# Kernel optimization log

Hardware: AMD Instinct MI355X
Metric: run time of the kernel (lower is better)

Reference implementation:

```python
import jax, jax.numpy as jnp
import numpy as np

N_NODES = 100000


def gcn_conv(x, W, b, src, dst, n):
    # PyG GCNConv: h = X @ W, add self-loops, symmetric normalization, scatter-add, + bias
    h = x @ W  # [N, out]
    loop = jnp.arange(n, dtype=src.dtype)
    src2 = jnp.concatenate([src, loop])
    dst2 = jnp.concatenate([dst, loop])
    ew = jnp.ones(src2.shape[0], dtype=h.dtype)
    deg = jax.ops.segment_sum(ew, dst2, num_segments=n)  # in-degree incl. self-loop
    dinv = jnp.where(deg > 0, jax.lax.rsqrt(deg), 0.0)
    norm = dinv[src2] * dinv[dst2]  # [E+N]
    msg = h[src2] * norm[:, None]  # gather + scale
    out = jax.ops.segment_sum(msg, dst2, num_segments=n)  # scatter-add
    return out + b


def setup_inputs() -> dict:
    key = jax.random.key(0)
    k1, k2, k3, k4, k5 = jax.random.split(key, 5)
    n, e = N_NODES, 3200000
    d_in, d_hid, d_out = 512, 16, 7
    x = jax.random.normal(k1, (n, d_in), dtype=jnp.float32)
    edge_index = jax.random.randint(k2, (2, e), 0, n, dtype=jnp.int64)
    W1 = jax.random.normal(k3, (d_in, d_hid), dtype=jnp.float32) / np.sqrt(d_in)
    b1 = jnp.zeros((d_hid,), dtype=jnp.float32)
    W2 = jax.random.normal(k4, (d_hid, d_out), dtype=jnp.float32) / np.sqrt(d_hid)
    b2 = jnp.zeros((d_out,), dtype=jnp.float32)
    return {"x": x, "edge_index": edge_index, "W1": W1, "b1": b1, "W2": W2, "b2": b2}


def reference(x, edge_index, W1, b1, W2, b2):
    n = x.shape[0]
    src, dst = edge_index[0], edge_index[1]
    h = jax.nn.relu(gcn_conv(x, W1, b1, src, dst, n))
    # dropout is identity in eval mode
    h = gcn_conv(h, W2, b2, src, dst, n)
    return jax.nn.log_softmax(h, axis=1)
```

## Files before the change

### kernel.cpp

```cpp
#include <hip/hip_runtime.h>
#include <math.h>

#define D_IN 512
#define F1   16
#define F2   7

#define BKT_SHIFT 8
#define PK_SHIFT  18
#define PK_MASK   ((1u << PK_SHIFT) - 1u)
#define A_CHUNK   8192
#define B_CAP     16384

typedef float vf4 __attribute__((ext_vector_type(4)));

__global__ __launch_bounds__(256) void binhist_kernel(const int* __restrict__ dst,
                                                      int* __restrict__ bucket_cnt,
                                                      int E, int NB) {
    __shared__ int lh[512];
    for (int i = threadIdx.x; i < 512; i += 256) lh[i] = 0;
    __syncthreads();
    int base = blockIdx.x * A_CHUNK;
#pragma unroll
    for (int i = 0; i < A_CHUNK / 256; ++i) {
        int t = base + i * 256 + threadIdx.x;
        if (t < E) {
            int d = __builtin_nontemporal_load(&dst[t]);
            atomicAdd(&lh[d >> BKT_SHIFT], 1);
        }
    }
    __syncthreads();
    for (int i = threadIdx.x; i < NB; i += 256) {
        int v = lh[i];
        if (v) atomicAdd(&bucket_cnt[i], v);
    }
}

__global__ __launch_bounds__(512) void bucketscan_kernel(const int* __restrict__ bucket_cnt,
                                                         int* __restrict__ bucket_base,
                                                         int* __restrict__ bucket_cursor,
                                                         int NB, int E) {
    __shared__ int sm[512];
    int tid = threadIdx.x;
    int v = (tid < NB) ? bucket_cnt[tid] : 0;
    sm[tid] = v;
    __syncthreads();
    for (int off = 1; off < 512; off <<= 1) {
        int t = (tid >= off) ? sm[tid - off] : 0;
        __syncthreads();
        sm[tid] += t;
        __syncthreads();
    }
    if (tid < NB) {
        int ex = sm[tid] - v;
        bucket_base[tid] = ex;
        bucket_cursor[tid] = ex;
    }
    if (tid == 0) bucket_base[NB] = E;
}

__global__ __launch_bounds__(256) void bin_kernel(const int* __restrict__ src,
                                                  const int* __restrict__ dst,
                                                  int* __restrict__ bucket_cursor,
                                                  unsigned int* __restrict__ binned,
                                                  int E, int NB) {
    __shared__ int lh[512];
    __shared__ int lbase[512];
    __shared__ int lcur[512];
    __shared__ int sdelta[512];
    __shared__ int sA[512], sB[512];
    __shared__ unsigned int rbuf[A_CHUNK];
    __shared__ int rdelta[A_CHUNK];
    int tid = threadIdx.x;
    for (int i = tid; i < 512; i += 256) lh[i] = 0;
    __syncthreads();

    int base = blockIdx.x * A_CHUNK;
    int dcache[A_CHUNK / 256];
    int scache[A_CHUNK / 256];
#pragma unroll
    for (int i = 0; i < A_CHUNK / 256; ++i) {
        int t = base + i * 256 + tid;
        int d = -1, s = 0;
        if (t < E) {
            d = __builtin_nontemporal_load(&dst[t]);
            s = __builtin_nontemporal_load(&src[t]);
            atomicAdd(&lh[d >> BKT_SHIFT], 1);
        }
        dcache[i] = d;
        scache[i] = s;
    }
    __syncthreads();

    for (int i = tid; i < 512; i += 256) sA[i] = lh[i];
    __syncthreads();
    int* psrc = sA; int* pdst = sB;
    for (int off = 1; off < 512; off <<= 1) {
        for (int i = tid; i < 512; i += 256)
            pdst[i] = psrc[i] + ((i >= off) ? psrc[i - off] : 0);
        __syncthreads();
        int* tmp = psrc; psrc = pdst; pdst = tmp;
    }
    for (int i = tid; i < 512; i += 256) {
        int ex = psrc[i] - lh[i];
        lbase[i] = ex;
        lcur[i] = ex;
    }
    __syncthreads();

    for (int b = tid; b < NB; b += 256) {
        int c = lh[b];
        int g = c ? atomicAdd(&bucket_cursor[b], c) : 0;
        sdelta[b] = g - lbase[b];
    }
    __syncthreads();

#pragma unroll
    for (int i = 0; i < A_CHUNK / 256; ++i) {
        int d = dcache[i];
        if (d >= 0) {
            int b = d >> BKT_SHIFT;
            int p = atomicAdd(&lcur[b], 1);
            rbuf[p] = (unsigned int)scache[i] | ((unsigned int)(d & 255) << PK_SHIFT);
            rdelta[p] = sdelta[b];
        }
    }
    __syncthreads();

    int total = min(A_CHUNK, E - base);
    for (int p = tid; p < total; p += 256)
        binned[rdelta[p] + p] = rbuf[p];
}

__global__ __launch_bounds__(256) void csr_kernel(const unsigned int* __restrict__ binned,
                                                  const int* __restrict__ bucket_base,
                                                  int* __restrict__ row_ptr,
                                                  int* __restrict__ row_end,
                                                  float* __restrict__ dinv,
                                                  int* __restrict__ adj, int n) {
    __shared__ int lh[256], lscan[256], lcur[256];
    __shared__ unsigned int rbuf[B_CAP];
    int b = blockIdx.x;
    int tid = threadIdx.x;
    int gbase = bucket_base[b];
    int gend  = bucket_base[b + 1];
    int m = gend - gbase;
    lh[tid] = 0;
    __syncthreads();
    for (int i = tid; i < m; i += 256) {
        unsigned int w = __builtin_nontemporal_load(&binned[gbase + i]);
        if (i < B_CAP) rbuf[i] = w;
        atomicAdd(&lh[w >> PK_SHIFT], 1);
    }
    __syncthreads();
    int v = lh[tid];
    lscan[tid] = v;
    __syncthreads();
    for (int off = 1; off < 256; off <<= 1) {
        int t = (tid >= off) ? lscan[tid - off] : 0;
        __syncthreads();
        lscan[tid] += t;
        __syncthreads();
    }
    int ex = lscan[tid] - v;
    int node = (b << BKT_SHIFT) + tid;
    if (node < n) {
        row_ptr[node] = gbase + ex;
        row_end[node] = gbase + ex + v;
        dinv[node] = rsqrtf((float)v + 1.0f);
    }
    lcur[tid] = ex;
    __syncthreads();
    for (int i = tid; i < m; i += 256) {
        unsigned int w = (i < B_CAP) ? rbuf[i] : binned[gbase + i];
        int d = (int)(w >> PK_SHIFT);
        int s = (int)(w & PK_MASK);
        int p = atomicAdd(&lcur[d], 1);
        adj[gbase + p] = s;
    }
}

__global__ __launch_bounds__(256, 2) void mm1_kernel(const float* __restrict__ x,
                                                     const float* __restrict__ W1,
                                                     const float* __restrict__ dinv,
                                                     float* __restrict__ h1s, int n) {
    int tid = threadIdx.x;
    int lane = tid & 63;
    int wid  = blockIdx.x * 4 + (tid >> 6);
    int nwaves = gridDim.x * 4;

    float wA[4][16], wB[4][16];
#pragma unroll
    for (int r = 0; r < 4; ++r) {
        const float4* ra = (const float4*)(W1 + (size_t)(4 * lane + r) * F1);
        const float4* rb = (const float4*)(W1 + (size_t)(256 + 4 * lane + r) * F1);
#pragma unroll
        for (int q = 0; q < 4; ++q) {
            float4 va = ra[q], vb = rb[q];
            wA[r][4 * q + 0] = va.x; wA[r][4 * q + 1] = va.y;
            wA[r][4 * q + 2] = va.z; wA[r][4 * q + 3] = va.w;
            wB[r][4 * q + 0] = vb.x; wB[r][4 * q + 1] = vb.y;
            wB[r][4 * q + 2] = vb.z; wB[r][4 * q + 3] = vb.w;
        }
    }

    int node = wid;
    if (node >= n) return;
    const float* xb = x + (size_t)node * D_IN;
    vf4 pA = *(const vf4*)(xb + 4 * lane);
    vf4 pB = *(const vf4*)(xb + 256 + 4 * lane);

    while (node < n) {
        vf4 xA = pA, xB = pB;
        int nx = node + nwaves;
        if (nx < n) {
            const float* xn = x + (size_t)nx * D_IN;
            pA = *(const vf4*)(xn + 4 * lane);
            pB = *(const vf4*)(xn + 256 + 4 * lane);
        }
        float acc[16];
#pragma unroll
        for (int f = 0; f < 16; ++f) acc[f] = 0.f;
#pragma unroll
        for (int r = 0; r < 4; ++r) {
            float ea = xA[r], eb = xB[r];
#pragma unroll
            for (int f = 0; f < 16; ++f) {
                acc[f] += ea * wA[r][f];
                acc[f] += eb * wB[r][f];
            }
        }
        int h0 = lane & 1, h1 = lane & 2, h2 = lane & 4, h3 = lane & 8;
        float a[8];
#pragma unroll
        for (int j = 0; j < 8; ++j) {
            float keep = h0 ? acc[2 * j + 1] : acc[2 * j];
            float give = h0 ? acc[2 * j] : acc[2 * j + 1];
            a[j] = keep + __shfl_xor(give, 1);
        }
        float b[4];
#pragma unroll
        for (int j = 0; j < 4; ++j) {
            float keep = h1 ? a[2 * j + 1] : a[2 * j];
            float give = h1 ? a[2 * j] : a[2 * j + 1];
            b[j] = keep + __shfl_xor(give, 2);
        }
        float c[2];
#pragma unroll
        for (int j = 0; j < 2; ++j) {
            float keep = h2 ? b[2 * j + 1] : b[2 * j];
            float give = h2 ? b[2 * j] : b[2 * j + 1];
            c[j] = keep + __shfl_xor(give, 4);
        }
        float d = (h3 ? c[1] : c[0]) + __shfl_xor(h3 ? c[0] : c[1], 8);
        d += __shfl_xor(d, 16);
        d += __shfl_xor(d, 32);
        if (lane < 16) {
            float di = dinv[node];
            h1s[(size_t)node * F1 + lane] = d * di;
        }
        node = nx;
    }
}

__global__ __launch_bounds__(256) void agg1_kernel(const int* __restrict__ row_ptr,
                                                   const int* __restrict__ row_end,
                                                   const int* __restrict__ adj,
                                                   const float* __restrict__ h,
                                                   const float* __restrict__ dinv,
                                                   const float* __restrict__ b1,
                                                   float* __restrict__ acc, int n) {
    int t = blockIdx.x * 256 + threadIdx.x;
    int node = t >> 4, j = t & 15;
    if (node >= n) return;
    int s = row_ptr[node], e = row_end[node];
    float a0 = 0.0f, a1 = 0.0f;
    int k = s;
    for (; k + 1 < e; k += 2) {
        int s0 = adj[k], s1 = adj[k + 1];
        a0 += h[(size_t)s0 * F1 + j];
        a1 += h[(size_t)s1 * F1 + j];
    }
    if (k < e) a0 += h[(size_t)adj[k] * F1 + j];
    float di = dinv[node];
    float v = di * (a0 + a1 + h[(size_t)node * F1 + j]) + b1[j];
    acc[(size_t)node * F1 + j] = v > 0.0f ? v : 0.0f;
}

__global__ __launch_bounds__(256) void mm2_kernel(const float* __restrict__ hin,
                                                  const float* __restrict__ W2,
                                                  const float* __restrict__ dinv,
                                                  float* __restrict__ h2s, int n) {
    int t = blockIdx.x * blockDim.x + threadIdx.x;
    if (t >= n) return;
    const float4* hr = (const float4*)(hin + (size_t)t * F1);
    float hv[F1];
#pragma unroll
    for (int q = 0; q < 4; ++q) {
        float4 v = hr[q];
        hv[4 * q + 0] = v.x; hv[4 * q + 1] = v.y;
        hv[4 * q + 2] = v.z; hv[4 * q + 3] = v.w;
    }
    float acc[F2];
#pragma unroll
    for (int j = 0; j < F2; ++j) acc[j] = 0.0f;
#pragma unroll
    for (int k = 0; k < F1; ++k) {
        float xv = hv[k];
#pragma unroll
        for (int j = 0; j < F2; ++j) acc[j] += xv * W2[k * F2 + j];
    }
    float di = dinv[t];
    float* outp = h2s + (size_t)t * 8;
#pragma unroll
    for (int j = 0; j < F2; ++j) outp[j] = acc[j] * di;
    outp[7] = 0.0f;
}

__global__ __launch_bounds__(256) void agg2_kernel(const int* __restrict__ row_ptr,
                                                   const int* __restrict__ row_end,
                                                   const int* __restrict__ adj,
                                                   const float* __restrict__ h,
                                                   const float* __restrict__ dinv,
                                                   const float* __restrict__ b2,
                                                   float* __restrict__ out, int n) {
    int t = blockIdx.x * 256 + threadIdx.x;
    int node = t >> 3, j = t & 7;
    if (node >= n) return;
    int s = row_ptr[node], e = row_end[node];
    float a0 = 0.0f, a1 = 0.0f;
    int k = s;
    for (; k + 1 < e; k += 2) {
        int s0 = adj[k], s1 = adj[k + 1];
        a0 += h[(size_t)s0 * 8 + j];
        a1 += h[(size_t)s1 * 8 + j];
    }
    if (k < e) a0 += h[(size_t)adj[k] * 8 + j];
    float di = dinv[node];
    float bj = j < F2 ? b2[j] : 0.0f;
    float v = di * (a0 + a1 + h[(size_t)node * 8 + j]) + bj;
    if (j >= F2) v = -INFINITY;
    float m = v;
#pragma unroll
    for (int w = 1; w < 8; w <<= 1) m = fmaxf(m, __shfl_xor(m, w, 8));
    float ex = (j < F2) ? expf(v - m) : 0.0f;
    float sum = ex;
#pragma unroll
    for (int w = 1; w < 8; w <<= 1) sum += __shfl_xor(sum, w, 8);
    float lse = m + logf(sum);
    if (j < F2) out[(size_t)node * F2 + j] = v - lse;
}

extern "C" void kernel_launch(void* const* d_in, const int* in_sizes, int n_in,
                              void* d_out, int out_size, void* d_ws, size_t ws_size,
                              hipStream_t stream) {
    const float* x  = (const float*)d_in[0];
    const int*   ei = (const int*)d_in[1];
    const float* W1 = (const float*)d_in[2];
    const float* b1 = (const float*)d_in[3];
    const float* W2 = (const float*)d_in[4];
    const float* b2 = (const float*)d_in[5];

    int n = in_sizes[0] / D_IN;
    int E = in_sizes[1] / 2;
    const int* src = ei;
    const int* dst = ei + E;
    int NB = (n + 255) >> BKT_SHIFT;

    char* ws = (char*)d_ws;
    size_t o = 0;
    int* bucket_cnt    = (int*)(ws + o); o += 512 * 4;
    int* bucket_base   = (int*)(ws + o); o += 516 * 4;
    int* bucket_cursor = (int*)(ws + o); o += 512 * 4;
    int*   row_ptr = (int*)(ws + o);   o += (size_t)n * 4;
    int*   row_end = (int*)(ws + o);   o += (size_t)n * 4;
    float* dinv    = (float*)(ws + o); o += (size_t)n * 4;
    int*   adj     = (int*)(ws + o);   o += (size_t)E * 4;
    size_t uni = (size_t)E > (size_t)n * 32 ? (size_t)E : (size_t)n * 32;
    unsigned int* binned = (unsigned int*)(ws + o);
    float* h1s  = (float*)(ws + o);
    float* acc1 = (float*)(ws + o) + (size_t)n * F1;
    o += uni * 4;
    float* h2s = h1s;
    float* out = (float*)d_out;

    const int B = 256;
    int GA = (E + A_CHUNK - 1) / A_CHUNK;
    int gN = (n + B - 1) / B;

    hipMemsetAsync(bucket_cnt, 0, 512 * sizeof(int), stream);

    binhist_kernel<<<GA, B, 0, stream>>>(dst, bucket_cnt, E, NB);
    bucketscan_kernel<<<1, 512, 0, stream>>>(bucket_cnt, bucket_base, bucket_cursor, NB, E);
    bin_kernel<<<GA, B, 0, stream>>>(src, dst, bucket_cursor, binned, E, NB);
    csr_kernel<<<NB, B, 0, stream>>>(binned, bucket_base, row_ptr, row_end, dinv, adj, n);

    mm1_kernel<<<512, B, 0, stream>>>(x, W1, dinv, h1s, n);

    agg1_kernel<<<((size_t)n * F1 + B - 1) / B, B, 0, stream>>>(row_ptr, row_end, adj, h1s, dinv, b1, acc1, n);

    mm2_kernel<<<gN, B, 0, stream>>>(acc1, W2, dinv, h2s, n);

    agg2_kernel<<<((size_t)n * 8 + B - 1) / B, B, 0, stream>>>(row_ptr, row_end, adj, h2s, dinv, b2, out, n);
}
```

Baseline: 500.9 us.

## Fuse layer-2 matmul into agg1 and vectorize neighbor gathers with float4

The layer-1 aggregation kernel now also applies bias, ReLU and the 16x7 W2 projection in registers, using lane shuffles to reduce partial products. The separate mm2 kernel and its intermediate buffer round trip are removed. Both aggregation kernels now split each node's edges across lane groups, with every lane loading a float4 slice of a neighbor row, followed by a shuffle reduction. This replaces scalar per-feature gathers and is meant to cut gather instruction count and raise memory-level parallelism. It costs extra shuffles, and lanes do uneven work when a node has few edges.

```diff
diff --git a/kernel.cpp b/kernel.cpp
--- a/kernel.cpp
+++ b/kernel.cpp
@@ -268,52 +268,58 @@
                                                    const float* __restrict__ h,
                                                    const float* __restrict__ dinv,
                                                    const float* __restrict__ b1,
-                                                   float* __restrict__ acc, int n) {
+                                                   const float* __restrict__ W2,
+                                                   float* __restrict__ h2s, int n) {
     int t = blockIdx.x * 256 + threadIdx.x;
-    int node = t >> 4, j = t & 15;
+    int node = t >> 4;
     if (node >= n) return;
+    int li = t & 15;
+    int jq = li & 3;
+    int e4 = li >> 2;
     int s = row_ptr[node], e = row_end[node];
-    float a0 = 0.0f, a1 = 0.0f;
-    int k = s;
-    for (; k + 1 < e; k += 2) {
-        int s0 = adj[k], s1 = adj[k + 1];
-        a0 += h[(size_t)s0 * F1 + j];
-        a1 += h[(size_t)s1 * F1 + j];
-    }
-    if (k < e) a0 += h[(size_t)adj[k] * F1 + j];
+    vf4 a0 = {0.f, 0.f, 0.f, 0.f}, a1 = {0.f, 0.f, 0.f, 0.f};
+    int k = s + e4;
+    for (; k + 4 < e; k += 8) {
+        int s0 = adj[k], s1 = adj[k + 4];
+        a0 += *(const vf4*)(h + (size_t)s0 * F1 + jq * 4);
+        a1 += *(const vf4*)(h + (size_t)s1 * F1 + jq * 4);
+    }
+    if (k < e) a0 += *(const vf4*)(h + (size_t)adj[k] * F1 + jq * 4);
+    vf4 sum = a0 + a1;
+#pragma unroll
+    for (int q = 0; q < 4; ++q) {
+        sum[q] += __shfl_xor(sum[q], 4, 16);
+        sum[q] += __shfl_xor(sum[q], 8, 16);
+    }
     float di = dinv[node];
-    float v = di * (a0 + a1 + h[(size_t)node * F1 + j]) + b1[j];
-    acc[(size_t)node * F1 + j] = v > 0.0f ? v : 0.0f;
-}
-
-__global__ __launch_bounds__(256) void mm2_kernel(const float* __restrict__ hin,
-                                                  const float* __restrict__ W2,
-                                                  const float* __restrict__ dinv,
-                                                  float* __restrict__ h2s, int n) {
-    int t = blockIdx.x * blockDim.x + threadIdx.x;
-    if (t >= n) return;
-    const float4* hr = (const float4*)(hin + (size_t)t * F1);
-    float hv[F1];
-#pragma unroll
-    for (int q = 0; q < 4; ++q) {
-        float4 v = hr[q];
-        hv[4 * q + 0] = v.x; hv[4 * q + 1] = v.y;
-        hv[4 * q + 2] = v.z; hv[4 * q + 3] = v.w;
-    }
-    float acc[F2];
-#pragma unroll
-    for (int j = 0; j < F2; ++j) acc[j] = 0.0f;
-#pragma unroll
-    for (int k = 0; k < F1; ++k) {
-        float xv = hv[k];
-#pragma unroll
-        for (int j = 0; j < F2; ++j) acc[j] += xv * W2[k * F2 + j];
-    }
-    float di = dinv[t];
-    float* outp = h2s + (size_t)t * 8;
-#pragma unroll
-    for (int j = 0; j < F2; ++j) outp[j] = acc[j] * di;
-    outp[7] = 0.0f;
+    vf4 self = *(const vf4*)(h + (size_t)node * F1 + jq * 4);
+    float v0 = di * (sum[0] + self[0]) + b1[jq * 4 + 0]; v0 = v0 > 0.f ? v0 : 0.f;
+    float v1 = di * (sum[1] + self[1]) + b1[jq * 4 + 1]; v1 = v1 > 0.f ? v1 : 0.f;
+    float v2 = di * (sum[2] + self[2]) + b1[jq * 4 + 2]; v2 = v2 > 0.f ? v2 : 0.f;
+    float v3 = di * (sum[3] + self[3]) + b1[jq * 4 + 3]; v3 = v3 > 0.f ? v3 : 0.f;
+    const float* w0 = W2 + (size_t)(jq * 4 + 0) * F2;
+    const float* w1 = W2 + (size_t)(jq * 4 + 1) * F2;
+    const float* w2 = W2 + (size_t)(jq * 4 + 2) * F2;
+    const float* w3 = W2 + (size_t)(jq * 4 + 3) * F2;
+    float p0 = v0 * w0[0] + v1 * w1[0] + v2 * w2[0] + v3 * w3[0];
+    float p1 = v0 * w0[1] + v1 * w1[1] + v2 * w2[1] + v3 * w3[1];
+    float p2 = v0 * w0[2] + v1 * w1[2] + v2 * w2[2] + v3 * w3[2];
+    float p3 = v0 * w0[3] + v1 * w1[3] + v2 * w2[3] + v3 * w3[3];
+    float p4 = v0 * w0[4] + v1 * w1[4] + v2 * w2[4] + v3 * w3[4];
+    float p5 = v0 * w0[5] + v1 * w1[5] + v2 * w2[5] + v3 * w3[5];
+    float p6 = v0 * w0[6] + v1 * w1[6] + v2 * w2[6] + v3 * w3[6];
+    p0 += __shfl_xor(p0, 1, 16); p0 += __shfl_xor(p0, 2, 16);
+    p1 += __shfl_xor(p1, 1, 16); p1 += __shfl_xor(p1, 2, 16);
+    p2 += __shfl_xor(p2, 1, 16); p2 += __shfl_xor(p2, 2, 16);
+    p3 += __shfl_xor(p3, 1, 16); p3 += __shfl_xor(p3, 2, 16);
+    p4 += __shfl_xor(p4, 1, 16); p4 += __shfl_xor(p4, 2, 16);
+    p5 += __shfl_xor(p5, 1, 16); p5 += __shfl_xor(p5, 2, 16);
+    p6 += __shfl_xor(p6, 1, 16); p6 += __shfl_xor(p6, 2, 16);
+    if (li < 8) {
+        float oc = li == 0 ? p0 : li == 1 ? p1 : li == 2 ? p2 : li == 3 ? p3
+                 : li == 4 ? p4 : li == 5 ? p5 : li == 6 ? p6 : 0.0f;
+        h2s[(size_t)node * 8 + li] = oc * di;
+    }
 }
 
 __global__ __launch_bounds__(256) void agg2_kernel(const int* __restrict__ row_ptr,
@@ -324,30 +330,40 @@
                                                    const float* __restrict__ b2,
                                                    float* __restrict__ out, int n) {
     int t = blockIdx.x * 256 + threadIdx.x;
-    int node = t >> 3, j = t & 7;
+    int node = t >> 3;
     if (node >= n) return;
+    int li = t & 7;
+    int jh = li & 1;
+    int e4 = li >> 1;
     int s = row_ptr[node], e = row_end[node];
-    float a0 = 0.0f, a1 = 0.0f;
-    int k = s;
-    for (; k + 1 < e; k += 2) {
-        int s0 = adj[k], s1 = adj[k + 1];
-        a0 += h[(size_t)s0 * 8 + j];
-        a1 += h[(size_t)s1 * 8 + j];
-    }
-    if (k < e) a0 += h[(size_t)adj[k] * 8 + j];
+    vf4 a0 = {0.f, 0.f, 0.f, 0.f}, a1 = {0.f, 0.f, 0.f, 0.f};
+    int k = s + e4;
+    for (; k + 4 < e; k += 8) {
+        int s0 = adj[k], s1 = adj[k + 4];
+        a0 += *(const vf4*)(h + (size_t)s0 * 8 + jh * 4);
+        a1 += *(const vf4*)(h + (size_t)s1 * 8 + jh * 4);
+    }
+    if (k < e) a0 += *(const vf4*)(h + (size_t)adj[k] * 8 + jh * 4);
+    vf4 sum = a0 + a1;
+#pragma unroll
+    for (int q = 0; q < 4; ++q) {
+        sum[q] += __shfl_xor(sum[q], 2, 8);
+        sum[q] += __shfl_xor(sum[q], 4, 8);
+    }
     float di = dinv[node];
-    float bj = j < F2 ? b2[j] : 0.0f;
-    float v = di * (a0 + a1 + h[(size_t)node * 8 + j]) + bj;
-    if (j >= F2) v = -INFINITY;
-    float m = v;
-#pragma unroll
-    for (int w = 1; w < 8; w <<= 1) m = fmaxf(m, __shfl_xor(m, w, 8));
-    float ex = (j < F2) ? expf(v - m) : 0.0f;
-    float sum = ex;
-#pragma unroll
-    for (int w = 1; w < 8; w <<= 1) sum += __shfl_xor(sum, w, 8);
-    float lse = m + logf(sum);
-    if (j < F2) out[(size_t)node * F2 + j] = v - lse;
+    vf4 self = *(const vf4*)(h + (size_t)node * 8 + jh * 4);
+    float v0 = di * (sum[0] + self[0]) + (jh ? b2[4] : b2[0]);
+    float v1 = di * (sum[1] + self[1]) + (jh ? b2[5] : b2[1]);
+    float v2 = di * (sum[2] + self[2]) + (jh ? b2[6] : b2[2]);
+    float v3 = jh ? -INFINITY : di * (sum[3] + self[3]) + b2[3];
+    float m4 = fmaxf(fmaxf(v0, v1), fmaxf(v2, v3));
+    float m = fmaxf(m4, __shfl_xor(m4, 1, 8));
+    float es = expf(v0 - m) + expf(v1 - m) + expf(v2 - m) + (jh ? 0.f : expf(v3 - m));
+    float ssum = es + __shfl_xor(es, 1, 8);
+    float lse = m + logf(ssum);
+    float* op = out + (size_t)node * F2 + jh * 4;
+    op[0] = v0 - lse; op[1] = v1 - lse; op[2] = v2 - lse;
+    if (!jh) op[3] = v3 - lse;
 }
 
 extern "C" void kernel_launch(void* const* d_in, const int* in_sizes, int n_in,
@@ -377,15 +393,13 @@
     int*   adj     = (int*)(ws + o);   o += (size_t)E * 4;
     size_t uni = (size_t)E > (size_t)n * 32 ? (size_t)E : (size_t)n * 32;
     unsigned int* binned = (unsigned int*)(ws + o);
-    float* h1s  = (float*)(ws + o);
-    float* acc1 = (float*)(ws + o) + (size_t)n * F1;
+    float* h1s = (float*)(ws + o);
+    float* h2s = (float*)(ws + o) + (size_t)n * F1;
     o += uni * 4;
-    float* h2s = h1s;
     float* out = (float*)d_out;
 
     const int B = 256;
     int GA = (E + A_CHUNK - 1) / A_CHUNK;
-    int gN = (n + B - 1) / B;
 
     hipMemsetAsync(bucket_cnt, 0, 512 * sizeof(int), stream);
 
@@ -396,9 +410,7 @@
 
     mm1_kernel<<<512, B, 0, stream>>>(x, W1, dinv, h1s, n);
 
-    agg1_kernel<<<((size_t)n * F1 + B - 1) / B, B, 0, stream>>>(row_ptr, row_end, adj, h1s, dinv, b1, acc1, n);
-
-    mm2_kernel<<<gN, B, 0, stream>>>(acc1, W2, dinv, h2s, n);
+    agg1_kernel<<<((size_t)n * F1 + B - 1) / B, B, 0, stream>>>(row_ptr, row_end, adj, h1s, dinv, b1, W2, h2s, n);
 
     agg2_kernel<<<((size_t)n * 8 + B - 1) / B, B, 0, stream>>>(row_ptr, row_end, adj, h2s, dinv, b2, out, n);
 }
```

Measured after the change: 471.2 us. -5.9%, faster.
